# Performance work log

Measured on AMD Instinct MI355X. Metric: run time of the kernel, lower is better.

## Reference

```python
import jax, jax.numpy as jnp
import numpy as np

B, T, C, NH = 1, 2048, 768, 12
HD = C // NH  # 64
BIAS_GATE = 1.0  # forward passes is_causal (True) into bias_gate slot; faithful to called path


def setup_inputs() -> dict:
    key = jax.random.key(0)
    k0, k1, k2 = jax.random.split(key, 3)
    s = 1.0 / np.sqrt(C).astype(np.float32)
    return {
        "x": jax.random.normal(k0, (B, T, C), jnp.float32),
        "W_attn": jax.random.normal(k1, (C, 3 * C), jnp.float32) * s,
        "b_attn": jnp.zeros((3 * C,), jnp.float32),
        "W_proj": jax.random.normal(k2, (C, C), jnp.float32) * s,
        "b_proj": jnp.zeros((C,), jnp.float32),
    }


def _sparse_attention(q, k, v):
    # q, k, v: [B, NH, T, HD]
    att = jnp.einsum("bhqd,bhkd->bhqk", q, k) * (1.0 / np.sqrt(HD).astype(np.float32))
    causal = jnp.tril(jnp.ones((T, T), dtype=bool))  # [T, T]
    att = jnp.where(causal[None, None], att, -jnp.inf)
    count = jnp.float32(T * (T + 1) / 2)  # tril mask sum

    att_gate = att + BIAS_GATE
    # gumbel_sample with sample=False: straight-through (hard > 0, sigmoid grad)
    sig = jax.nn.sigmoid(att_gate)
    edge_samples = (att_gate > 0).astype(att.dtype) + sig - jax.lax.stop_gradient(sig)

    sm_att = jax.nn.softmax(att, axis=-1)
    y = jnp.einsum("bhqk,bhkd->bhqd", sm_att * edge_samples, v)
    l1 = sig.sum(axis=(-1, -2)) / count  # [B, NH]
    adj = att_gate > 0  # bool [B, NH, T, T]
    return y, l1, adj


def reference(x, W_attn, b_attn, W_proj, b_proj):
    qkv = x @ W_attn + b_attn  # [B, T, 3C]
    q, k, v = jnp.split(qkv, 3, axis=-1)

    def to_heads(t):
        return t.reshape(B, T, NH, HD).transpose(0, 2, 1, 3)  # [B, NH, T, HD]

    y, l1, adj = _sparse_attention(to_heads(q), to_heads(k), to_heads(v))
    y = y.transpose(0, 2, 1, 3).reshape(B, T, C)  # merge heads
    y = y @ W_proj + b_proj  # dropout rate = 0.0 (eval)
    return (y, adj)
```

## Files before the change

### kernel.cpp

```cpp
#include <hip/hip_runtime.h>
#include <math.h>

#define T_SEQ 2048
#define C_DIM 768
#define NH_N  12
#define HD_N  64
#define N3_DIM 2304

typedef __attribute__((ext_vector_type(8))) short s8v;
typedef __attribute__((ext_vector_type(4))) float f4v;

__device__ __forceinline__ ushort f2bf(float x) {
  const unsigned u = __float_as_uint(x);
  return (ushort)((u + 0x7FFFu + ((u >> 16) & 1u)) >> 16);
}

__global__ __launch_bounds__(256)
void gemm_chunk(const float* __restrict__ A, const float* __restrict__ B,
                float* __restrict__ CmBase, float* __restrict__ part,
                const int M, const int N, const int K,
                const int c0, const int c1, const int c2, const int c3) {
  const int bnd[4] = {c0, c1, c2, c3};
  const int z = blockIdx.z, nz = gridDim.z;
  const int kbeg = bnd[z], kend = bnd[z + 1];
  float* __restrict__ Cm = (z == nz - 1) ? CmBase : part + (size_t)z * M * N;

  __shared__ float As[2][16 * 64];
  __shared__ float Bs[2][16][128];
  const int tid = threadIdx.x;
  const int bm = blockIdx.y, bn = blockIdx.x;
  const int ty = tid >> 4, tx = tid & 15;
  const int arow = tid >> 2;
  const int acol = (tid & 3) << 2;
  const int brow = tid >> 4;
  const int bcol = (tid & 15) << 3;
  const int b3 = tid & 3;
  const int swA = (b3 << 2) | ((b3 & 1) << 4);

  const float* Ap = A + (size_t)(bm * 64 + arow) * K + acol;
  const float* Bp = B + (size_t)brow * N + bn * 128 + bcol;

  float acc[4][8];
#pragma unroll
  for (int i = 0; i < 4; ++i)
#pragma unroll
    for (int j = 0; j < 8; ++j) acc[i][j] = 0.f;

  float4 av = *(const float4*)(Ap + kbeg);
  float4 bv0 = *(const float4*)(Bp + (size_t)kbeg * N);
  float4 bv1 = *(const float4*)(Bp + (size_t)kbeg * N + 4);

  As[0][(acol + 0) * 64 + (arow ^ swA)] = av.x;
  As[0][(acol + 1) * 64 + (arow ^ swA)] = av.y;
  As[0][(acol + 2) * 64 + (arow ^ swA)] = av.z;
  As[0][(acol + 3) * 64 + (arow ^ swA)] = av.w;
  *(float4*)&Bs[0][brow][bcol] = bv0;
  *(float4*)&Bs[0][brow][bcol + 4] = bv1;
  __syncthreads();

  int p = 0;
  for (int k0 = kbeg; k0 < kend; k0 += 16) {
    const bool more = (k0 + 16 < kend);
    if (more) {
      av = *(const float4*)(Ap + k0 + 16);
      bv0 = *(const float4*)(Bp + (size_t)(k0 + 16) * N);
      bv1 = *(const float4*)(Bp + (size_t)(k0 + 16) * N + 4);
    }
#pragma unroll
    for (int kk = 0; kk < 16; ++kk) {
      const int kb = kk >> 2;
      const int swr = (kb << 2) | ((kb & 1) << 4);
      const float4 a = *(const float4*)&As[p][kk * 64 + ((ty * 4) ^ swr)];
      const float4 b0 = *(const float4*)&Bs[p][kk][tx * 4];
      const float4 b1 = *(const float4*)&Bs[p][kk][64 + tx * 4];
      const float aa[4] = {a.x, a.y, a.z, a.w};
      const float bb[8] = {b0.x, b0.y, b0.z, b0.w, b1.x, b1.y, b1.z, b1.w};
#pragma unroll
      for (int i = 0; i < 4; ++i)
#pragma unroll
        for (int j = 0; j < 8; ++j)
          acc[i][j] = fmaf(aa[i], bb[j], acc[i][j]);
    }
    if (more) {
      const int q = p ^ 1;
      As[q][(acol + 0) * 64 + (arow ^ swA)] = av.x;
      As[q][(acol + 1) * 64 + (arow ^ swA)] = av.y;
      As[q][(acol + 2) * 64 + (arow ^ swA)] = av.z;
      As[q][(acol + 3) * 64 + (arow ^ swA)] = av.w;
      *(float4*)&Bs[q][brow][bcol] = bv0;
      *(float4*)&Bs[q][brow][bcol + 4] = bv1;
      __syncthreads();
      p = q;
    }
  }

  const int crow = bm * 64 + ty * 4;
  const int ccol = bn * 128 + tx * 4;
#pragma unroll
  for (int i = 0; i < 4; ++i) {
    float4 o0, o1;
    o0.x = acc[i][0]; o0.y = acc[i][1]; o0.z = acc[i][2]; o0.w = acc[i][3];
    o1.x = acc[i][4]; o1.y = acc[i][5]; o1.z = acc[i][6]; o1.w = acc[i][7];
    *(float4*)&Cm[(size_t)(crow + i) * N + ccol] = o0;
    *(float4*)&Cm[(size_t)(crow + i) * N + ccol + 64] = o1;
  }
}

__global__ __launch_bounds__(256)
void gemm_join(float* __restrict__ Cm, const float* __restrict__ part,
               const float* __restrict__ bias, const int N,
               const size_t total4, const int nparts, const size_t partstride) {
  for (size_t i = blockIdx.x * 256 + threadIdx.x; i < total4;
       i += (size_t)gridDim.x * 256) {
    const size_t e = i * 4;
    float4 s = *(const float4*)&part[e];
    if (nparts > 1) {
      const float4 p1 = *(const float4*)&part[partstride + e];
      s.x += p1.x; s.y += p1.y; s.z += p1.z; s.w += p1.w;
    }
    const float4 c = *(const float4*)&Cm[e];
    s.x += c.x; s.y += c.y; s.z += c.z; s.w += c.w;
    const int col = (int)(e % N);
    const float4 b = *(const float4*)&bias[col];
    s.x += b.x; s.y += b.y; s.z += b.z; s.w += b.w;
    *(float4*)&Cm[e] = s;
  }
}

#define LOADKV(KB)                                                              \
  {                                                                             \
    _Pragma("unroll")                                                           \
    for (int l = 0; l < 4; ++l) {                                               \
      const int f = tid + l * 256;                                              \
      const int j = f >> 4, d4 = (f & 15) << 2;                                 \
      kreg[l] = *(const float4*)(qkv + (size_t)((KB) * 64 + j) * N3_DIM + C_DIM + h * HD_N + d4); \
      vreg[l] = *(const float4*)(qkv + (size_t)((KB) * 64 + j) * N3_DIM + 2 * C_DIM + h * HD_N + d4); \
    }                                                                           \
  }

__global__ __launch_bounds__(256)
void attn_part(const float* __restrict__ qkv, float* __restrict__ y_att,
               float* __restrict__ adj, float* __restrict__ ypart,
               float* __restrict__ lpart) {
#pragma clang fp contract(off)
  const int h  = blockIdx.y;
  const int tid = threadIdx.x;
  const int ty = tid >> 4, tx = tid & 15;
  const int ty4 = ty * 4, tx4 = tx * 4;
  const int w  = ty >> 2;
  const int lw = tid & 63;

  int qb = 0, c = blockIdx.x;
#pragma unroll 1
  for (; qb < 32; ++qb) { const int n = (qb + 6) / 6; if (c < n) break; c -= n; }
  const int nt = qb + 1;
  const int nc = (qb + 6) / 6;
  const int kb0 = (c * nt) / nc;
  const int kb1 = ((c + 1) * nt) / nc;
  const int t0 = qb * 64;

  __shared__ __align__(16) float  QsT[64 * 64];
  __shared__ __align__(16) float  KP[64 * 64];
  __shared__ __align__(16) ushort VT[4096];

  if (c == 0) {
    const int c0 = (qb + 1) * 64;
    const int W4 = (T_SEQ - c0) >> 2;
    const float4 z = make_float4(0.f, 0.f, 0.f, 0.f);
    for (int r = 0; r < 64; ++r) {
      float4* dst = (float4*)(adj + ((size_t)h * T_SEQ + t0 + r) * T_SEQ + c0);
      for (int cc = tid; cc < W4; cc += 256) dst[cc] = z;
    }
  }

#pragma unroll
  for (int l = 0; l < 4; ++l) {
    const int f = tid + l * 256;
    const int i = f >> 4, d4 = (f & 15) << 2;
    const float4 v = *(const float4*)(qkv + (size_t)(t0 + i) * N3_DIM + h * HD_N + d4);
    const int cq = i ^ d4;
    QsT[(d4 + 0) * 64 + cq] = v.x; QsT[(d4 + 1) * 64 + cq] = v.y;
    QsT[(d4 + 2) * 64 + cq] = v.z; QsT[(d4 + 3) * 64 + cq] = v.w;
  }

  float l_run[4];
  f4v yacc[4];
#pragma unroll
  for (int ii = 0; ii < 4; ++ii) {
    l_run[ii] = 0.f;
    yacc[ii] = (f4v){0.f, 0.f, 0.f, 0.f};
  }

  float4 kreg[4], vreg[4];
  LOADKV(kb0)

  for (int kb = kb0; kb < kb1; ++kb) {
    __syncthreads();
#pragma unroll
    for (int l = 0; l < 4; ++l) {
      const int f = tid + l * 256;
      const int j = f >> 4, d4 = (f & 15) << 2;
      const int ck = j ^ d4;
      KP[(d4 + 0) * 64 + ck] = kreg[l].x; KP[(d4 + 1) * 64 + ck] = kreg[l].y;
      KP[(d4 + 2) * 64 + ck] = kreg[l].z; KP[(d4 + 3) * 64 + ck] = kreg[l].w;
      const int jsV = j >> 5, gV = (j >> 3) & 3, eV = j & 7;
      const float vv[4] = {vreg[l].x, vreg[l].y, vreg[l].z, vreg[l].w};
#pragma unroll
      for (int k = 0; k < 4; ++k) {
        const int d = d4 + k;
        const int R = (d >> 4) * 2 + jsV;
        const int slot = gV * 16 + (d & 15);
        const int phys = slot ^ (slot >> 3) ^ R;
        VT[R * 512 + phys * 8 + eV] = f2bf(vv[k]);
      }
    }
    __syncthreads();
    if (kb + 1 < kb1) LOADKV(kb + 1)

    float acc[4][4];
#pragma unroll
    for (int ii = 0; ii < 4; ++ii)
#pragma unroll
      for (int jj = 0; jj < 4; ++jj) acc[ii][jj] = 0.f;
#pragma unroll 16
    for (int d = 0; d < 64; ++d) {
      const int sw = d & 60;
      const float4 qv = *(const float4*)&QsT[d * 64 + (ty4 ^ sw)];
      const float4 kv = *(const float4*)&KP[d * 64 + (tx4 ^ sw)];
      const float qa[4] = {qv.x, qv.y, qv.z, qv.w};
      const float ka[4] = {kv.x, kv.y, kv.z, kv.w};
#pragma unroll
      for (int ii = 0; ii < 4; ++ii)
#pragma unroll
        for (int jj = 0; jj < 4; ++jj)
          acc[ii][jj] = fmaf(qa[ii], ka[jj], acc[ii][jj]);
    }

    float pe[4][4];
#pragma unroll
    for (int ii = 0; ii < 4; ++ii) {
      const int ig = t0 + ty4 + ii;
      float rs = 0.f;
      float4 ev;
      float* evp = &ev.x;
#pragma unroll
      for (int jj = 0; jj < 4; ++jj) {
        const int jg = kb * 64 + tx4 + jj;
        if (jg <= ig) {
          const float t = acc[ii][jj] * 0.125f;
          const float g = t + 1.0f;
          const bool eg = (g > 0.0f);
          const float pp = __expf(t - 8.0f);
          rs += pp;
          pe[ii][jj] = eg ? pp : 0.f;
          evp[jj] = eg ? 1.0f : 0.0f;
        } else {
          pe[ii][jj] = 0.f;
          evp[jj] = 0.f;
        }
      }
      l_run[ii] += rs;
      *(float4*)(adj + ((size_t)h * T_SEQ + ig) * T_SEQ + kb * 64 + tx4) = ev;
    }

    __syncthreads();
    {
      ushort* Pb = (ushort*)KP;
      const int jsP = tx >> 3;
      const int gP = (tx & 7) >> 1;
      const int ebase = (tx & 1) << 2;
      const int R = w * 2 + jsP;
#pragma unroll
      for (int ii = 0; ii < 4; ++ii) {
        const int i15 = (ty4 + ii) & 15;
        const int slot = gP * 16 + i15;
        const int phys = slot ^ (slot >> 3) ^ R;
        const unsigned p01 = (unsigned)f2bf(pe[ii][0]) | ((unsigned)f2bf(pe[ii][1]) << 16);
        const unsigned p23 = (unsigned)f2bf(pe[ii][2]) | ((unsigned)f2bf(pe[ii][3]) << 16);
        *(uint2*)&Pb[R * 512 + phys * 8 + ebase] = make_uint2(p01, p23);
      }
    }
    __syncthreads();

    {
      const ushort* Pb = (const ushort*)KP;
      const int lsw = lw ^ (lw >> 3);
#pragma unroll
      for (int js = 0; js < 2; ++js) {
        const int RP = w * 2 + js;
        const s8v pa = *(const s8v*)&Pb[RP * 512 + (lsw ^ RP) * 8];
#pragma unroll
        for (int dblk = 0; dblk < 4; ++dblk) {
          const int RV = dblk * 2 + js;
          const s8v vb = *(const s8v*)&VT[RV * 512 + (lsw ^ RV) * 8];
          yacc[dblk] = __builtin_amdgcn_mfma_f32_16x16x32_bf16(pa, vb, yacc[dblk], 0, 0, 0);
        }
      }
    }
  }

#pragma unroll
  for (int ii = 0; ii < 4; ++ii)
#pragma unroll
    for (int off = 1; off < 16; off <<= 1)
      l_run[ii] += __shfl_xor(l_run[ii], off, 16);

  if (nc == 1) {
#pragma unroll
    for (int reg = 0; reg < 4; ++reg) {
      const float inv = 1.0f / l_run[reg];
      const int row = t0 + ty4 + reg;
#pragma unroll
      for (int dblk = 0; dblk < 4; ++dblk)
        y_att[(size_t)row * C_DIM + h * HD_N + dblk * 16 + tx] = yacc[dblk][reg] * inv;
    }
  } else {
    int pidx = 0;
#pragma unroll 1
    for (int q = 6; q < qb; ++q) pidx += (q + 6) / 6;
    const int s = h * 96 + pidx + c;
    if (tx == 0) {
#pragma unroll
      for (int ii = 0; ii < 4; ++ii)
        lpart[(size_t)s * 64 + ty4 + ii] = l_run[ii];
    }
#pragma unroll
    for (int reg = 0; reg < 4; ++reg) {
      const int row = ty4 + reg;
#pragma unroll
      for (int dblk = 0; dblk < 4; ++dblk)
        ypart[(size_t)s * 4096 + row * 64 + dblk * 16 + tx] = yacc[dblk][reg];
    }
  }
}

__global__ __launch_bounds__(256)
void attn_combine(const float* __restrict__ ypart,
                  const float* __restrict__ lpart, float* __restrict__ y_att) {
  const int qb = 6 + blockIdx.x;
  const int h  = blockIdx.y;
  const int tid = threadIdx.x;
  const int nc = (qb + 6) / 6;
  int pidx = 0;
#pragma unroll 1
  for (int q = 6; q < qb; ++q) pidx += (q + 6) / 6;
  const int s0 = h * 96 + pidx;

  const int i  = tid >> 2;
  const int dq = tid & 3;

  float lstar = 0.f;
  for (int c = 0; c < nc; ++c)
    lstar += lpart[(size_t)(s0 + c) * 64 + i];
  const float inv = 1.0f / lstar;

#pragma unroll
  for (int e = 0; e < 4; ++e) {
    const int d = dq * 16 + e * 4;
    float4 a = make_float4(0.f, 0.f, 0.f, 0.f);
    for (int c = 0; c < nc; ++c) {
      const float4 p = *(const float4*)&ypart[(size_t)(s0 + c) * 4096 + i * 64 + d];
      a.x += p.x; a.y += p.y; a.z += p.z; a.w += p.w;
    }
    a.x *= inv; a.y *= inv; a.z *= inv; a.w *= inv;
    *(float4*)(y_att + (size_t)(qb * 64 + i) * C_DIM + h * HD_N + d) = a;
  }
}

extern "C" void kernel_launch(void* const* d_in, const int* in_sizes, int n_in,
                              void* d_out, int out_size, void* d_ws, size_t ws_size,
                              hipStream_t stream) {
  const float* x      = (const float*)d_in[0];
  const float* W_attn = (const float*)d_in[1];
  const float* b_attn = (const float*)d_in[2];
  const float* W_proj = (const float*)d_in[3];
  const float* b_proj = (const float*)d_in[4];

  float* y_out   = (float*)d_out;
  float* adj_out = y_out + (size_t)T_SEQ * C_DIM;

  float* partA = (float*)d_ws;
  float* qkv   = partA + (size_t)1152 * 4096;
  float* y_att = qkv + (size_t)T_SEQ * N3_DIM;
  float* lprt  = y_att + (size_t)T_SEQ * C_DIM;

  gemm_chunk<<<dim3(N3_DIM / 128, T_SEQ / 64, 2), 256, 0, stream>>>(
      x, W_attn, qkv, partA, T_SEQ, N3_DIM, C_DIM, 0, 512, 768, 0);
  gemm_join<<<1024, 256, 0, stream>>>(
      qkv, partA, b_attn, N3_DIM, (size_t)T_SEQ * N3_DIM / 4, 1, 0);

  attn_part<<<dim3(102, NH_N), 256, 0, stream>>>(qkv, y_att, adj_out, partA, lprt);
  attn_combine<<<dim3(26, NH_N), 256, 0, stream>>>(partA, lprt, y_att);

  gemm_chunk<<<dim3(C_DIM / 128, T_SEQ / 64, 3), 256, 0, stream>>>(
      y_att, W_proj, y_out, partA, T_SEQ, C_DIM, C_DIM, 0, 256, 512, 768);
  gemm_join<<<512, 256, 0, stream>>>(
      y_out, partA, b_proj, C_DIM, (size_t)T_SEQ * C_DIM / 4, 2,
      (size_t)T_SEQ * C_DIM);
}
```

Measured before the change: 263.2 us.

## Compute V projection with bf16 MFMA and rebalance attention query-block splitting

The V third of the QKV projection moves out of the fp32 split-K SIMT GEMM into a new bf16 MFMA kernel that adds the bias directly. The fp32 GEMM and its join kernel now handle only the Q and K columns, using separate leading dimensions. Attention splitting also changes from one chunk per six key blocks to one per five, giving more partial blocks (119 per head) and a larger partial workspace. Rounding V to bf16 lowers its precision and may affect accuracy.

```diff
diff --git a/kernel.cpp b/kernel.cpp
--- a/kernel.cpp
+++ b/kernel.cpp
@@ -18,12 +18,14 @@
 __global__ __launch_bounds__(256)
 void gemm_chunk(const float* __restrict__ A, const float* __restrict__ B,
                 float* __restrict__ CmBase, float* __restrict__ part,
-                const int M, const int N, const int K,
+                const int ldb, const int Nout, const int K, const int ldc,
                 const int c0, const int c1, const int c2, const int c3) {
   const int bnd[4] = {c0, c1, c2, c3};
   const int z = blockIdx.z, nz = gridDim.z;
   const int kbeg = bnd[z], kend = bnd[z + 1];
-  float* __restrict__ Cm = (z == nz - 1) ? CmBase : part + (size_t)z * M * N;
+  const bool fin = (z == nz - 1);
+  float* __restrict__ Cm = fin ? CmBase : part + (size_t)z * T_SEQ * Nout;
+  const int ost = fin ? ldc : Nout;
 
   __shared__ float As[2][16 * 64];
   __shared__ float Bs[2][16][128];
@@ -38,7 +40,7 @@
   const int swA = (b3 << 2) | ((b3 & 1) << 4);
 
   const float* Ap = A + (size_t)(bm * 64 + arow) * K + acol;
-  const float* Bp = B + (size_t)brow * N + bn * 128 + bcol;
+  const float* Bp = B + (size_t)brow * ldb + bn * 128 + bcol;
 
   float acc[4][8];
 #pragma unroll
@@ -47,8 +49,8 @@
     for (int j = 0; j < 8; ++j) acc[i][j] = 0.f;
 
   float4 av = *(const float4*)(Ap + kbeg);
-  float4 bv0 = *(const float4*)(Bp + (size_t)kbeg * N);
-  float4 bv1 = *(const float4*)(Bp + (size_t)kbeg * N + 4);
+  float4 bv0 = *(const float4*)(Bp + (size_t)kbeg * ldb);
+  float4 bv1 = *(const float4*)(Bp + (size_t)kbeg * ldb + 4);
 
   As[0][(acol + 0) * 64 + (arow ^ swA)] = av.x;
   As[0][(acol + 1) * 64 + (arow ^ swA)] = av.y;
@@ -63,8 +65,8 @@
     const bool more = (k0 + 16 < kend);
     if (more) {
       av = *(const float4*)(Ap + k0 + 16);
-      bv0 = *(const float4*)(Bp + (size_t)(k0 + 16) * N);
-      bv1 = *(const float4*)(Bp + (size_t)(k0 + 16) * N + 4);
+      bv0 = *(const float4*)(Bp + (size_t)(k0 + 16) * ldb);
+      bv1 = *(const float4*)(Bp + (size_t)(k0 + 16) * ldb + 4);
     }
 #pragma unroll
     for (int kk = 0; kk < 16; ++kk) {
@@ -101,29 +103,88 @@
     float4 o0, o1;
     o0.x = acc[i][0]; o0.y = acc[i][1]; o0.z = acc[i][2]; o0.w = acc[i][3];
     o1.x = acc[i][4]; o1.y = acc[i][5]; o1.z = acc[i][6]; o1.w = acc[i][7];
-    *(float4*)&Cm[(size_t)(crow + i) * N + ccol] = o0;
-    *(float4*)&Cm[(size_t)(crow + i) * N + ccol + 64] = o1;
+    *(float4*)&Cm[(size_t)(crow + i) * ost + ccol] = o0;
+    *(float4*)&Cm[(size_t)(crow + i) * ost + ccol + 64] = o1;
   }
 }
 
 __global__ __launch_bounds__(256)
 void gemm_join(float* __restrict__ Cm, const float* __restrict__ part,
-               const float* __restrict__ bias, const int N,
+               const float* __restrict__ bias, const int N, const int ldc,
                const size_t total4, const int nparts, const size_t partstride) {
   for (size_t i = blockIdx.x * 256 + threadIdx.x; i < total4;
        i += (size_t)gridDim.x * 256) {
     const size_t e = i * 4;
+    const int row = (int)(e / N);
+    const int col = (int)(e % N);
     float4 s = *(const float4*)&part[e];
     if (nparts > 1) {
       const float4 p1 = *(const float4*)&part[partstride + e];
       s.x += p1.x; s.y += p1.y; s.z += p1.z; s.w += p1.w;
     }
-    const float4 c = *(const float4*)&Cm[e];
+    float* dst = &Cm[(size_t)row * ldc + col];
+    const float4 c = *(const float4*)dst;
     s.x += c.x; s.y += c.y; s.z += c.z; s.w += c.w;
-    const int col = (int)(e % N);
     const float4 b = *(const float4*)&bias[col];
     s.x += b.x; s.y += b.y; s.z += b.z; s.w += b.w;
-    *(float4*)&Cm[e] = s;
+    *(float4*)dst = s;
+  }
+}
+
+__global__ __launch_bounds__(256)
+void gemm_v_mfma(const float* __restrict__ A, const float* __restrict__ W,
+                 const float* __restrict__ bias, float* __restrict__ Cv) {
+  const int tid = threadIdx.x;
+  const int bn = blockIdx.x, bm = blockIdx.y;
+  const int w = tid >> 6, lw = tid & 63;
+
+  __shared__ __align__(16) ushort Af[4096];
+  __shared__ __align__(16) ushort Bf[4096];
+
+  f4v acc[4];
+#pragma unroll
+  for (int nb = 0; nb < 4; ++nb) acc[nb] = (f4v){0.f, 0.f, 0.f, 0.f};
+
+  const int r = tid >> 2;
+  const int q4 = (tid & 3) << 4;
+
+  for (int k0 = 0; k0 < C_DIM; k0 += 64) {
+    __syncthreads();
+#pragma unroll
+    for (int u = 0; u < 4; ++u) {
+      const int kk = q4 + u * 4;
+      const float4 a = *(const float4*)&A[(size_t)(bm * 64 + r) * C_DIM + k0 + kk];
+      const float4 b = *(const float4*)&W[(size_t)(k0 + r) * N3_DIM + 1536 + bn * 64 + kk];
+      const float aa[4] = {a.x, a.y, a.z, a.w};
+      const float bb[4] = {b.x, b.y, b.z, b.w};
+#pragma unroll
+      for (int e4 = 0; e4 < 4; ++e4) {
+        const int k = kk + e4;
+        Af[(((r >> 4) * 2) + (k >> 5)) * 512 + ((((k >> 3) & 3) << 4) + (r & 15)) * 8 + (k & 7)] = f2bf(aa[e4]);
+        Bf[(((k >> 4) * 2) + (r >> 5)) * 512 + ((((r >> 3) & 3) << 4) + (k & 15)) * 8 + (r & 7)] = f2bf(bb[e4]);
+      }
+    }
+    __syncthreads();
+#pragma unroll
+    for (int js = 0; js < 2; ++js) {
+      const s8v pa = *(const s8v*)&Af[(w * 2 + js) * 512 + lw * 8];
+#pragma unroll
+      for (int nb = 0; nb < 4; ++nb) {
+        const s8v vb = *(const s8v*)&Bf[(nb * 2 + js) * 512 + lw * 8];
+        acc[nb] = __builtin_amdgcn_mfma_f32_16x16x32_bf16(pa, vb, acc[nb], 0, 0, 0);
+      }
+    }
+  }
+
+#pragma unroll
+  for (int nb = 0; nb < 4; ++nb) {
+    const int col = bn * 64 + nb * 16 + (lw & 15);
+    const float bv = bias[col];
+#pragma unroll
+    for (int reg = 0; reg < 4; ++reg) {
+      const int row = bm * 64 + w * 16 + ((lw >> 4) << 2) + reg;
+      Cv[(size_t)row * N3_DIM + 1536 + col] = acc[nb][reg] + bv;
+    }
   }
 }
 
@@ -152,9 +213,9 @@
 
   int qb = 0, c = blockIdx.x;
 #pragma unroll 1
-  for (; qb < 32; ++qb) { const int n = (qb + 6) / 6; if (c < n) break; c -= n; }
+  for (; qb < 32; ++qb) { const int n = (qb + 5) / 5; if (c < n) break; c -= n; }
   const int nt = qb + 1;
-  const int nc = (qb + 6) / 6;
+  const int nc = (qb + 5) / 5;
   const int kb0 = (c * nt) / nc;
   const int kb1 = ((c + 1) * nt) / nc;
   const int t0 = qb * 64;
@@ -317,8 +378,8 @@
   } else {
     int pidx = 0;
 #pragma unroll 1
-    for (int q = 6; q < qb; ++q) pidx += (q + 6) / 6;
-    const int s = h * 96 + pidx + c;
+    for (int q = 5; q < qb; ++q) pidx += (q + 5) / 5;
+    const int s = h * 114 + pidx + c;
     if (tx == 0) {
 #pragma unroll
       for (int ii = 0; ii < 4; ++ii)
@@ -337,14 +398,14 @@
 __global__ __launch_bounds__(256)
 void attn_combine(const float* __restrict__ ypart,
                   const float* __restrict__ lpart, float* __restrict__ y_att) {
-  const int qb = 6 + blockIdx.x;
+  const int qb = 5 + blockIdx.x;
   const int h  = blockIdx.y;
   const int tid = threadIdx.x;
-  const int nc = (qb + 6) / 6;
+  const int nc = (qb + 5) / 5;
   int pidx = 0;
 #pragma unroll 1
-  for (int q = 6; q < qb; ++q) pidx += (q + 6) / 6;
-  const int s0 = h * 96 + pidx;
+  for (int q = 5; q < qb; ++q) pidx += (q + 5) / 5;
+  const int s0 = h * 114 + pidx;
 
   const int i  = tid >> 2;
   const int dq = tid & 3;
@@ -380,21 +441,23 @@
   float* adj_out = y_out + (size_t)T_SEQ * C_DIM;
 
   float* partA = (float*)d_ws;
-  float* qkv   = partA + (size_t)1152 * 4096;
+  float* qkv   = partA + (size_t)1368 * 4096;
   float* y_att = qkv + (size_t)T_SEQ * N3_DIM;
   float* lprt  = y_att + (size_t)T_SEQ * C_DIM;
 
-  gemm_chunk<<<dim3(N3_DIM / 128, T_SEQ / 64, 2), 256, 0, stream>>>(
-      x, W_attn, qkv, partA, T_SEQ, N3_DIM, C_DIM, 0, 512, 768, 0);
+  gemm_chunk<<<dim3(12, T_SEQ / 64, 2), 256, 0, stream>>>(
+      x, W_attn, qkv, partA, N3_DIM, 1536, C_DIM, N3_DIM, 0, 512, 768, 0);
+  gemm_v_mfma<<<dim3(12, 32), 256, 0, stream>>>(
+      x, W_attn, b_attn + 1536, qkv);
   gemm_join<<<1024, 256, 0, stream>>>(
-      qkv, partA, b_attn, N3_DIM, (size_t)T_SEQ * N3_DIM / 4, 1, 0);
-
-  attn_part<<<dim3(102, NH_N), 256, 0, stream>>>(qkv, y_att, adj_out, partA, lprt);
-  attn_combine<<<dim3(26, NH_N), 256, 0, stream>>>(partA, lprt, y_att);
+      qkv, partA, b_attn, 1536, N3_DIM, (size_t)T_SEQ * 1536 / 4, 1, 0);
+
+  attn_part<<<dim3(119, NH_N), 256, 0, stream>>>(qkv, y_att, adj_out, partA, lprt);
+  attn_combine<<<dim3(27, NH_N), 256, 0, stream>>>(partA, lprt, y_att);
 
   gemm_chunk<<<dim3(C_DIM / 128, T_SEQ / 64, 3), 256, 0, stream>>>(
-      y_att, W_proj, y_out, partA, T_SEQ, C_DIM, C_DIM, 0, 256, 512, 768);
+      y_att, W_proj, y_out, partA, C_DIM, C_DIM, C_DIM, C_DIM, 0, 256, 512, 768);
   gemm_join<<<512, 256, 0, stream>>>(
-      y_out, partA, b_proj, C_DIM, (size_t)T_SEQ * C_DIM / 4, 2,
+      y_out, partA, b_proj, C_DIM, C_DIM, (size_t)T_SEQ * C_DIM / 4, 2,
       (size_t)T_SEQ * C_DIM);
 }
```

New measurement: 245.6 us. 6.7% less time.
